# Optimization experiments

Measured on AMD Instinct MI355X. Metric: run time of the kernel, lower is better.

Reference implementation:

```python
import jax, jax.numpy as jnp
import numpy as np


def setup_inputs() -> dict:
    key = jax.random.key(0)
    N, nH, D, L, P = 2, 8, 32, 4, 4
    shapes = np.array([[92, 92], [46, 46], [23, 23], [12, 12]], dtype=np.int64)
    areas = shapes[:, 0] * shapes[:, 1]
    Lin = int(areas.sum())  # 11253
    Lq = Lin  # encoder self-attention
    k1, k2, k3 = jax.random.split(key, 3)
    value = jax.random.normal(k1, (N, Lin, nH, D), dtype=jnp.float32)
    sampling_locations = jax.random.uniform(k2, (N, Lq, nH, L, P, 2), dtype=jnp.float32)
    aw = jax.random.uniform(k3, (N, Lq, nH, L, P), dtype=jnp.float32)
    attention_weights = aw / aw.sum(axis=(-2, -1), keepdims=True)  # softmax-normalized over L*P
    spatial_shapes = jnp.asarray(shapes)
    starts = np.concatenate([[0], np.cumsum(areas)[:-1]])
    level_start_index = jnp.asarray(starts, dtype=jnp.int64)
    return dict(value=value, spatial_shapes=spatial_shapes,
                level_start_index=level_start_index,
                sampling_locations=sampling_locations,
                attention_weights=attention_weights)


def _gather2d(v_nh, xi, yi, Hl, Wl):
    # v_nh: [N, nH, Hl*Wl, D]; xi, yi: [N, Lq, nH, P] int32 pixel coords
    N, Lq, nH, P = xi.shape
    valid = (xi >= 0) & (xi < Wl) & (yi >= 0) & (yi < Hl)
    xc = jnp.clip(xi, 0, Wl - 1)
    yc = jnp.clip(yi, 0, Hl - 1)
    idx = (yc * Wl + xc).transpose(0, 2, 1, 3).reshape(N, nH, Lq * P)
    vals = jax.vmap(jax.vmap(lambda v, i: v[i]))(v_nh, idx)  # [N, nH, Lq*P, D]
    vals = vals.reshape(N, nH, Lq, P, -1).transpose(0, 2, 1, 3, 4)  # [N, Lq, nH, P, D]
    return vals * valid[..., None].astype(vals.dtype)


def reference(value, spatial_shapes, level_start_index, sampling_locations, attention_weights):
    # ms_deform_attn core: per-level bilinear sampling (align_corners=False,
    # zero padding) at learned locations, weighted sum over levels and points.
    shapes_np = np.asarray(spatial_shapes)
    starts_np = np.asarray(level_start_index)
    N, Lin, nH, D = value.shape
    _, Lq, _, L, P, _ = sampling_locations.shape
    out = jnp.zeros((N, Lq, nH, D), dtype=value.dtype)
    for lvl in range(L):
        Hl, Wl = int(shapes_np[lvl, 0]), int(shapes_np[lvl, 1])
        s = int(starts_np[lvl])
        v_nh = value[:, s:s + Hl * Wl].transpose(0, 2, 1, 3)  # [N, nH, Hl*Wl, D]
        loc = sampling_locations[:, :, :, lvl]  # [N, Lq, nH, P, 2]
        # grid_sample convention: normalized [0,1] -> pixel coord, align_corners=False
        x = loc[..., 0] * Wl - 0.5
        y = loc[..., 1] * Hl - 0.5
        x0f = jnp.floor(x); y0f = jnp.floor(y)
        dx = x - x0f; dy = y - y0f
        x0 = x0f.astype(jnp.int32); y0 = y0f.astype(jnp.int32)
        x1 = x0 + 1; y1 = y0 + 1
        w00 = ((1.0 - dx) * (1.0 - dy))[..., None]
        w01 = (dx * (1.0 - dy))[..., None]
        w10 = ((1.0 - dx) * dy)[..., None]
        w11 = (dx * dy)[..., None]
        samp = (w00 * _gather2d(v_nh, x0, y0, Hl, Wl)
                + w01 * _gather2d(v_nh, x1, y0, Hl, Wl)
                + w10 * _gather2d(v_nh, x0, y1, Hl, Wl)
                + w11 * _gather2d(v_nh, x1, y1, Hl, Wl))  # [N, Lq, nH, P, D]
        aw_l = attention_weights[:, :, :, lvl]  # [N, Lq, nH, P]
        out = out + (samp * aw_l[..., None]).sum(axis=3)
    return out.reshape(N, Lq, nH * D)
```

## Files before the change

kernel.cpp:

```cpp
#include <hip/hip_runtime.h>

#define NH 8
#define DD 32
#define LL 4
#define PP 4

typedef float  f32x4  __attribute__((ext_vector_type(4)));
typedef float  f32x2  __attribute__((ext_vector_type(2)));
typedef int    i32x4  __attribute__((ext_vector_type(4)));
typedef _Float16 half4v __attribute__((ext_vector_type(4)));

__global__ __launch_bounds__(256) void conv_kernel(
    const float* __restrict__ value, _Float16* __restrict__ vh,
    int Lin, int total)
{
    int tid = blockIdx.x * blockDim.x + threadIdx.x;
    if (tid >= total) return;
    const int d4  = tid & 7;
    const int pos = (tid >> 3) % Lin;
    const int nh  = tid / (8 * Lin);
    const int n   = nh >> 3;
    const int h   = nh & 7;

    const f32x4 v = *(const f32x4*)(value + (((size_t)n * Lin + pos) * NH + h) * DD + d4 * 4);
    half4v o;
    o.x = (_Float16)v.x; o.y = (_Float16)v.y; o.z = (_Float16)v.z; o.w = (_Float16)v.w;
    *(half4v*)(vh + ((size_t)nh * Lin + pos) * DD + d4 * 4) = o;
}

#define FMAMIX_LO(ACC, DW, W) \
    asm("v_fma_mix_f32 %0, %1, %2, %0 op_sel:[0,0,0] op_sel_hi:[1,0,0]" \
        : "+v"(ACC) : "v"(DW), "v"(W))
#define FMAMIX_HI(ACC, DW, W) \
    asm("v_fma_mix_f32 %0, %1, %2, %0 op_sel:[1,0,0] op_sel_hi:[1,0,0]" \
        : "+v"(ACC) : "v"(DW), "v"(W))

__global__ __attribute__((amdgpu_flat_work_group_size(256, 256)))
__attribute__((amdgpu_waves_per_eu(4)))
void msda_fwd_h(
    const _Float16* __restrict__ vh,
    const int*   __restrict__ ssh,
    const int*   __restrict__ lsi,
    const float* __restrict__ sloc,
    const float* __restrict__ aw,
    float*       __restrict__ out,
    int N, int Lq, int Lin, int spx, int nSlabs)
{
    __shared__ i32x4 ent[32 * 41];

    const int xcd   = blockIdx.x & 7;
    const int blk   = blockIdx.x >> 3;
    const int sw    = blk % spx;
    const int chunk = blk / spx;
    const int slab  = xcd * spx + sw;
    if (slab >= nSlabs) return;

    const int t  = threadIdx.x;
    const int u  = t >> 3;
    const int j  = t & 7;
    const int q  = chunk * 32 + u;
    const int qc = min(q, Lq - 1);
    const int n  = slab >> 3;
    const int h  = slab & 7;

    {
        const size_t nqh = ((size_t)n * Lq + qc) * NH + h;
        const int l = j >> 1;
        const bool is64 = (ssh[1] == 0);
        const int W = is64 ? ssh[4 * l + 2] : ssh[2 * l + 1];
        const int H = is64 ? ssh[4 * l]     : ssh[2 * l];
        const int S = is64 ? lsi[2 * l]     : lsi[l];
        const f32x4 lc = __builtin_nontemporal_load((const f32x4*)sloc + nqh * 8 + j);
        const f32x2 av = __builtin_nontemporal_load((const f32x2*)aw + nqh * 8 + j);
        const float fW = (float)W, fH = (float)H;
        const int rowb  = W * (DD * 2);
        const int sbase = S * (DD * 2);
#pragma unroll
        for (int pt = 0; pt < 2; ++pt) {
            const float x  = lc[2 * pt]     * fW - 0.5f;
            const float y  = lc[2 * pt + 1] * fH - 0.5f;
            const float wq = av[pt];
            const float x0f = floorf(x), y0f = floorf(y);
            const int x0 = (int)x0f, y0 = (int)y0f;
            const float dx = x - x0f, dy = y - y0f;
            const int x1 = x0 + 1, y1 = y0 + 1;
            const bool vx0 = (x0 >= 0) & (x0 < W), vx1 = (x1 >= 0) & (x1 < W);
            const bool vy0 = (y0 >= 0) & (y0 < H), vy1 = (y1 >= 0) & (y1 < H);
            const int cx0 = min(max(x0, 0), W - 1), cx1 = min(max(x1, 0), W - 1);
            const int cy0 = min(max(y0, 0), H - 1), cy1 = min(max(y1, 0), H - 1);
            const float wx0 = (1.f - dx) * wq * (vx0 ? 1.f : 0.f);
            const float wx1 = dx         * wq * (vx1 ? 1.f : 0.f);
            const float ty  = (1.f - dy) * (vy0 ? 1.f : 0.f);
            const float by  = dy         * (vy1 ? 1.f : 0.f);
            const int rt = cy0 * rowb + sbase;
            const int rb = cy1 * rowb + sbase;
            i32x4 e0, e1;
            e0.x = rt + cx0 * (DD * 2);  e0.y = rb + cx0 * (DD * 2);
            e0.z = __float_as_int(wx0 * ty);  e0.w = __float_as_int(wx0 * by);
            e1.x = rt + cx1 * (DD * 2);  e1.y = rb + cx1 * (DD * 2);
            e1.z = __float_as_int(wx1 * ty);  e1.w = __float_as_int(wx1 * by);
            const int base = u * 41 + 5 * j + 2 * pt;
            ent[base]     = e0;
            ent[base + 1] = e1;
        }
    }
    __syncthreads();
    if (q >= Lq) return;

    const int side = j >> 2;
    const int cg   = j & 3;
    const char* __restrict__ sb =
        (const char*)vh + (size_t)slab * Lin * (DD * 2) + cg * 16;
    const int ub = u * 41 + side;

    float acc[8];
#pragma unroll
    for (int k = 0; k < 8; ++k) acc[k] = 0.f;

#define RD(b, E) { \
    E[0] = ent[ub + 10 * (b) + 0]; \
    E[1] = ent[ub + 10 * (b) + 2]; \
    E[2] = ent[ub + 10 * (b) + 5]; \
    E[3] = ent[ub + 10 * (b) + 7]; }
#define LD(E, V) _Pragma("unroll") \
    for (int i = 0; i < 4; ++i) { \
        V[2*i]   = *(const i32x4*)(sb + (unsigned)E[i].x); \
        V[2*i+1] = *(const i32x4*)(sb + (unsigned)E[i].y); }
#define AC(E, V) _Pragma("unroll") \
    for (int i = 0; i < 4; ++i) { \
        const float wt = __int_as_float(E[i].z); \
        const float wb = __int_as_float(E[i].w); \
        _Pragma("unroll") for (int d = 0; d < 4; ++d) { \
            FMAMIX_LO(acc[2*d],   V[2*i][d],   wt); \
            FMAMIX_HI(acc[2*d+1], V[2*i][d],   wt); \
            FMAMIX_LO(acc[2*d],   V[2*i+1][d], wb); \
            FMAMIX_HI(acc[2*d+1], V[2*i+1][d], wb); } }

    i32x4 E0[4], E1[4], E2[4], E3[4];
    i32x4 V0[8], V1[8], V2[8], V3[8];
    RD(0, E0) LD(E0, V0)
    RD(1, E1) LD(E1, V1)
    AC(E0, V0)
    RD(2, E2) LD(E2, V2)
    AC(E1, V1)
    RD(3, E3) LD(E3, V3)
    AC(E2, V2)
    AC(E3, V3)

#pragma unroll
    for (int k = 0; k < 8; ++k)
        acc[k] += __shfl_xor(acc[k], 4);

    f32x4 st;
    st.x = acc[side * 4 + 0];
    st.y = acc[side * 4 + 1];
    st.z = acc[side * 4 + 2];
    st.w = acc[side * 4 + 3];
    const size_t onqh = ((size_t)n * Lq + q) * NH + h;
    __builtin_nontemporal_store(st, (f32x4*)(out + onqh * DD + cg * 8 + side * 4));
}

__global__ __launch_bounds__(256) void msda_fwd_f32(
    const float* __restrict__ value,
    const int*   __restrict__ spatial_shapes,
    const int*   __restrict__ level_start,
    const float* __restrict__ sloc,
    const float* __restrict__ aw,
    float*       __restrict__ out,
    int N, int Lq, int Lin, int total)
{
    int tid = blockIdx.x * blockDim.x + threadIdx.x;
    if (tid >= total) return;
    const int c  = tid & 7;
    const int h  = (tid >> 3) & 7;
    const int nq = tid >> 6;
    const int n  = nq / Lq;
    const bool is64 = (spatial_shapes[1] == 0);
    int Hs[LL], Ws[LL], Ss[LL];
#pragma unroll
    for (int l = 0; l < LL; ++l) {
        if (is64) { Hs[l] = spatial_shapes[4*l]; Ws[l] = spatial_shapes[4*l+2]; Ss[l] = level_start[2*l]; }
        else      { Hs[l] = spatial_shapes[2*l]; Ws[l] = spatial_shapes[2*l+1]; Ss[l] = level_start[l]; }
    }
    const size_t nqh = (size_t)nq * NH + h;
    const float* loc_p = sloc + nqh * (LL * PP * 2);
    const float* aw_p  = aw   + nqh * (LL * PP);
    float4 acc = make_float4(0.f, 0.f, 0.f, 0.f);
#pragma unroll
    for (int l = 0; l < LL; ++l) {
        const int H = Hs[l], W = Ws[l];
        const float* vb = value + (((size_t)n * Lin + Ss[l]) * NH + h) * DD + c * 4;
#pragma unroll
        for (int p = 0; p < PP; ++p) {
            const int jj = l * PP + p;
            const float x = loc_p[2*jj] * (float)W - 0.5f;
            const float y = loc_p[2*jj+1] * (float)H - 0.5f;
            const float w = aw_p[jj];
            const float x0f = floorf(x), y0f = floorf(y);
            const int x0 = (int)x0f, y0 = (int)y0f, x1 = x0+1, y1 = y0+1;
            const float dx = x - x0f, dy = y - y0f;
            const bool vx0 = x0>=0 && x0<W, vx1 = x1>=0 && x1<W;
            const bool vy0 = y0>=0 && y0<H, vy1 = y1>=0 && y1<H;
            const int cx0 = min(max(x0,0),W-1), cx1 = min(max(x1,0),W-1);
            const int cy0 = min(max(y0,0),H-1), cy1 = min(max(y1,0),H-1);
            const float w00 = (1.f-dx)*(1.f-dy)*w*((vx0&&vy0)?1.f:0.f);
            const float w01 = dx*(1.f-dy)*w*((vx1&&vy0)?1.f:0.f);
            const float w10 = (1.f-dx)*dy*w*((vx0&&vy1)?1.f:0.f);
            const float w11 = dx*dy*w*((vx1&&vy1)?1.f:0.f);
            const float4 v00 = *(const float4*)(vb + (size_t)(cy0*W+cx0)*(NH*DD));
            const float4 v01 = *(const float4*)(vb + (size_t)(cy0*W+cx1)*(NH*DD));
            const float4 v10 = *(const float4*)(vb + (size_t)(cy1*W+cx0)*(NH*DD));
            const float4 v11 = *(const float4*)(vb + (size_t)(cy1*W+cx1)*(NH*DD));
            acc.x += w00*v00.x + w01*v01.x + w10*v10.x + w11*v11.x;
            acc.y += w00*v00.y + w01*v01.y + w10*v10.y + w11*v11.y;
            acc.z += w00*v00.z + w01*v01.z + w10*v10.z + w11*v11.z;
            acc.w += w00*v00.w + w01*v01.w + w10*v10.w + w11*v11.w;
        }
    }
    *(float4*)(out + nqh * DD + c * 4) = acc;
}

extern "C" void kernel_launch(void* const* d_in, const int* in_sizes, int n_in,
                              void* d_out, int out_size, void* d_ws, size_t ws_size,
                              hipStream_t stream)
{
    const float* value = (const float*)d_in[0];
    const int*   ss    = (const int*)  d_in[1];
    const int*   lsi   = (const int*)  d_in[2];
    const float* sloc  = (const float*)d_in[3];
    const float* aw    = (const float*)d_in[4];
    float* out = (float*)d_out;

    const int N = 2;
    const int Lq  = in_sizes[4] / (N * NH * LL * PP);
    const int Lin = in_sizes[0] / (N * NH * DD);

    const size_t need = (size_t)N * NH * Lin * DD * sizeof(_Float16);
    if (ws_size >= need) {
        _Float16* vh = (_Float16*)d_ws;
        const int ctotal = N * NH * Lin * 8;
        conv_kernel<<<(ctotal + 255) / 256, 256, 0, stream>>>(value, vh, Lin, ctotal);

        const int nSlabs = N * NH;
        const int spx    = (nSlabs + 7) / 8;
        const int chunks = (Lq + 31) / 32;
        const int grid   = 8 * spx * chunks;
        msda_fwd_h<<<grid, 256, 0, stream>>>(vh, ss, lsi, sloc, aw, out,
                                             N, Lq, Lin, spx, nSlabs);
    } else {
        const int total = N * Lq * NH * 8;
        msda_fwd_f32<<<(total + 255) / 256, 256, 0, stream>>>(value, ss, lsi, sloc, aw, out,
                                                              N, Lq, Lin, total);
    }
}
```

Baseline: 135.0 us.

## Stage coarse pyramid levels of value slab into LDS for bilinear gathers

Each block now cooperatively copies the two smallest feature levels of its (batch, head) slab into a ~43KB shared-memory buffer. Gathers for those levels then read from LDS instead of global memory, and level 2/3 entry reads are hoisted ahead of the accumulation. This targets scattered global/L2 gather traffic for the coarse levels. In exchange, every block pays a full coalesced copy for only 32 queries, and the large LDS footprint cuts occupancy. The waves_per_eu hint is also dropped.

```diff
diff --git a/kernel.cpp b/kernel.cpp
--- a/kernel.cpp
+++ b/kernel.cpp
@@ -4,6 +4,8 @@
 #define DD 32
 #define LL 4
 #define PP 4
+#define PXB (DD * 2)
+#define STAGE_BYTES 43264
 
 typedef float  f32x4  __attribute__((ext_vector_type(4)));
 typedef float  f32x2  __attribute__((ext_vector_type(2)));
@@ -36,7 +38,6 @@
         : "+v"(ACC) : "v"(DW), "v"(W))
 
 __global__ __attribute__((amdgpu_flat_work_group_size(256, 256)))
-__attribute__((amdgpu_waves_per_eu(4)))
 void msda_fwd_h(
     const _Float16* __restrict__ vh,
     const int*   __restrict__ ssh,
@@ -47,6 +48,7 @@
     int N, int Lq, int Lin, int spx, int nSlabs)
 {
     __shared__ i32x4 ent[32 * 41];
+    __shared__ __align__(16) char stage[STAGE_BYTES];
 
     const int xcd   = blockIdx.x & 7;
     const int blk   = blockIdx.x >> 3;
@@ -63,18 +65,35 @@
     const int n  = slab >> 3;
     const int h  = slab & 7;
 
+    const bool is64 = (ssh[1] == 0);
+    const int H2 = is64 ? ssh[8]  : ssh[4];
+    const int W2 = is64 ? ssh[10] : ssh[5];
+    const int H3 = is64 ? ssh[12] : ssh[6];
+    const int W3 = is64 ? ssh[14] : ssh[7];
+    const int S2 = is64 ? lsi[4]  : lsi[2];
+    const int stBytes = (H2 * W2 + H3 * W3) * PXB;
+    const bool staged = (stBytes <= STAGE_BYTES);
+
+    const char* __restrict__ slabBase = (const char*)vh + (size_t)slab * Lin * PXB;
+
+    if (staged) {
+        const char* __restrict__ src = slabBase + (size_t)S2 * PXB;
+        const int nch = stBytes >> 4;
+        for (int i = t; i < nch; i += 256)
+            *(i32x4*)(stage + (size_t)i * 16) = *(const i32x4*)(src + (size_t)i * 16);
+    }
+
     {
         const size_t nqh = ((size_t)n * Lq + qc) * NH + h;
         const int l = j >> 1;
-        const bool is64 = (ssh[1] == 0);
         const int W = is64 ? ssh[4 * l + 2] : ssh[2 * l + 1];
         const int H = is64 ? ssh[4 * l]     : ssh[2 * l];
         const int S = is64 ? lsi[2 * l]     : lsi[l];
         const f32x4 lc = __builtin_nontemporal_load((const f32x4*)sloc + nqh * 8 + j);
         const f32x2 av = __builtin_nontemporal_load((const f32x2*)aw + nqh * 8 + j);
         const float fW = (float)W, fH = (float)H;
-        const int rowb  = W * (DD * 2);
-        const int sbase = S * (DD * 2);
+        const int rowb  = W * PXB;
+        const int sbase = (staged && l >= 2) ? (S - S2) * PXB : S * PXB;
 #pragma unroll
         for (int pt = 0; pt < 2; ++pt) {
             const float x  = lc[2 * pt]     * fW - 0.5f;
@@ -95,9 +114,9 @@
             const int rt = cy0 * rowb + sbase;
             const int rb = cy1 * rowb + sbase;
             i32x4 e0, e1;
-            e0.x = rt + cx0 * (DD * 2);  e0.y = rb + cx0 * (DD * 2);
+            e0.x = rt + cx0 * PXB;  e0.y = rb + cx0 * PXB;
             e0.z = __float_as_int(wx0 * ty);  e0.w = __float_as_int(wx0 * by);
-            e1.x = rt + cx1 * (DD * 2);  e1.y = rb + cx1 * (DD * 2);
+            e1.x = rt + cx1 * PXB;  e1.y = rb + cx1 * PXB;
             e1.z = __float_as_int(wx1 * ty);  e1.w = __float_as_int(wx1 * by);
             const int base = u * 41 + 5 * j + 2 * pt;
             ent[base]     = e0;
@@ -109,8 +128,8 @@
 
     const int side = j >> 2;
     const int cg   = j & 3;
-    const char* __restrict__ sb =
-        (const char*)vh + (size_t)slab * Lin * (DD * 2) + cg * 16;
+    const int cg16 = cg * 16;
+    const char* __restrict__ sb = slabBase + cg16;
     const int ub = u * 41 + side;
 
     float acc[8];
@@ -126,6 +145,10 @@
     for (int i = 0; i < 4; ++i) { \
         V[2*i]   = *(const i32x4*)(sb + (unsigned)E[i].x); \
         V[2*i+1] = *(const i32x4*)(sb + (unsigned)E[i].y); }
+#define LDL(E, V) _Pragma("unroll") \
+    for (int i = 0; i < 4; ++i) { \
+        V[2*i]   = *(const i32x4*)(stage + (unsigned)(E[i].x + cg16)); \
+        V[2*i+1] = *(const i32x4*)(stage + (unsigned)(E[i].y + cg16)); }
 #define AC(E, V) _Pragma("unroll") \
     for (int i = 0; i < 4; ++i) { \
         const float wt = __int_as_float(E[i].z); \
@@ -140,10 +163,11 @@
     i32x4 V0[8], V1[8], V2[8], V3[8];
     RD(0, E0) LD(E0, V0)
     RD(1, E1) LD(E1, V1)
+    RD(2, E2) RD(3, E3)
+    if (staged) { LDL(E2, V2) LDL(E3, V3) }
+    else        { LD(E2, V2)  LD(E3, V3)  }
     AC(E0, V0)
-    RD(2, E2) LD(E2, V2)
     AC(E1, V1)
-    RD(3, E3) LD(E3, V3)
     AC(E2, V2)
     AC(E3, V3)
 
```

Measured after the change: 160.0 us. +18.5%, slower.
